# Optimization experiments

Measured on AMD Instinct MI355X. Metric: run time of the kernel, lower is better.

The kernel has to match this reference:

```python
import jax, jax.numpy as jnp
import numpy as np

B, T, TS, J, D, H = 4, 512, 512, 17, 256, 8
CD = D // H
SCALE = CD ** -0.5


def setup_inputs() -> dict:
    key = jax.random.key(0)
    ks = jax.random.split(key, 7)
    return {
        "q": jax.random.normal(ks[0], (B, T, J, D), dtype=jnp.float32),
        "kv": jax.random.normal(ks[1], (B, TS, J, D), dtype=jnp.float32),
        "Wq": jax.random.normal(ks[2], (D, D), dtype=jnp.float32) * (D ** -0.5),
        "Wk": jax.random.normal(ks[3], (D, D), dtype=jnp.float32) * (D ** -0.5),
        "Wv": jax.random.normal(ks[4], (D, D), dtype=jnp.float32) * (D ** -0.5),
        "Wp": jax.random.normal(ks[5], (D, D), dtype=jnp.float32) * (D ** -0.5),
        "bp": jnp.zeros((D,), dtype=jnp.float32),
    }


def reference(q, kv, Wq, Wk, Wv, Wp, bp):
    b, t, j, d = q.shape
    t_sup = kv.shape[1]
    h, cd = H, CD
    # linear projections (torch Linear: x @ W^T), split heads -> [b,h,j,t,cd]
    qh = (q @ Wq.T).reshape(b, t, j, h, cd).transpose(0, 3, 2, 1, 4)
    kh = (kv @ Wk.T).reshape(b, t_sup, j, h, cd).transpose(0, 3, 2, 1, 4)
    vh = (kv @ Wv.T).reshape(b, t_sup, j, h, cd).transpose(0, 3, 2, 1, 4)
    # full attention matrix over temporal axes: [b,h,j,t,t_sup]
    scores = jnp.einsum("bhjtc,bhjsc->bhjts", qh, kh) * SCALE
    attn = jax.nn.softmax(scores, axis=-1)
    out = jnp.einsum("bhjts,bhjsc->bhjtc", attn, vh)
    out = out.transpose(0, 3, 2, 1, 4).reshape(b, t, j, d)  # [b,t,j,d]
    return out @ Wp.T + bp
```

## Files before the change

### kernel.cpp

```cpp
#include <hip/hip_runtime.h>
#include <hip/hip_bf16.h>

#define BB 4
#define TT 512
#define JJ 17
#define DD 256
#define HH 8
#define MROWS (BB*TT*JJ)
#define SZE ((size_t)MROWS * DD)
#define WSZ (DD*DD)
#define QSCALE 0.2550265247510319f

typedef short v8s __attribute__((ext_vector_type(8)));
typedef float v4f __attribute__((ext_vector_type(4)));

__device__ __forceinline__ unsigned short f2bf(float f) {
    union { float f; unsigned int u; } c; c.f = f;
    unsigned int u = c.u;
    return (unsigned short)((u + 0x7FFF + ((u >> 16) & 1)) >> 16);
}
__device__ __forceinline__ unsigned int pkbf(float lo, float hi) {
    union { float f; unsigned int u; } a, b; a.f = lo; b.f = hi;
    return __builtin_amdgcn_perm(b.u + 0x8000u, a.u + 0x8000u, 0x07060302u);
}

__global__ __launch_bounds__(256) void prep_kernel(
    const float* __restrict__ q, const float* __restrict__ kv,
    const float* __restrict__ Wq, const float* __restrict__ Wk,
    const float* __restrict__ Wv, const float* __restrict__ Wp,
    unsigned short* __restrict__ qb, unsigned short* __restrict__ kvb,
    unsigned short* __restrict__ Wqb, unsigned short* __restrict__ Wkb,
    unsigned short* __restrict__ Wvb, unsigned short* __restrict__ Wpb)
{
    size_t i = ((size_t)blockIdx.x * 256 + threadIdx.x) * 8;
    const float* src; unsigned short* dst; size_t off; float scale = 1.f;
    if (i < SZE)            { src = q;  dst = qb;  off = i;        scale = QSCALE; }
    else if (i < 2 * SZE)   { src = kv; dst = kvb; off = i - SZE; }
    else {
        size_t k = i - 2 * SZE;
        int w = (int)(k >> 16);
        off = k & (WSZ - 1);
        src = (w == 0) ? Wq : (w == 1) ? Wk : (w == 2) ? Wv : Wp;
        dst = (w == 0) ? Wqb : (w == 1) ? Wkb : (w == 2) ? Wvb : Wpb;
    }
    float4 x0 = *(const float4*)(src + off);
    float4 x1 = *(const float4*)(src + off + 4);
    union { unsigned short s[8]; int4 v; } u;
    u.s[0] = f2bf(x0.x * scale); u.s[1] = f2bf(x0.y * scale);
    u.s[2] = f2bf(x0.z * scale); u.s[3] = f2bf(x0.w * scale);
    u.s[4] = f2bf(x1.x * scale); u.s[5] = f2bf(x1.y * scale);
    u.s[6] = f2bf(x1.z * scale); u.s[7] = f2bf(x1.w * scale);
    *(int4*)(dst + off) = u.v;
}

__global__ __launch_bounds__(256) void gemm_kernel(
    const unsigned short* __restrict__ A0,
    const unsigned short* __restrict__ A1,
    const unsigned short* __restrict__ A2,
    const unsigned short* __restrict__ W0,
    const unsigned short* __restrict__ W1,
    const unsigned short* __restrict__ W2,
    unsigned short* __restrict__ Y0,
    unsigned short* __restrict__ Y1,
    unsigned short* __restrict__ Y2,
    const float* __restrict__ bias,
    float* __restrict__ outf,
    int fp32out)
{
    const int z = blockIdx.z;
    const unsigned short* A = (z == 0) ? A0 : (z == 1) ? A1 : A2;
    const unsigned short* W = (z == 0) ? W0 : (z == 1) ? W1 : W2;
    unsigned short* Y       = (z == 0) ? Y0 : (z == 1) ? Y1 : Y2;

    const int bm = blockIdx.x;
    const int bn = blockIdx.y;

    __shared__ unsigned short As[128 * 40];
    __shared__ unsigned short Bs[128 * 40];

    const int tid  = threadIdx.x;
    const int wave = tid >> 6;
    const int lane = tid & 63;
    const int wm   = wave & 1;
    const int wn   = wave >> 1;
    const int quad = lane >> 4;
    const int l16  = lane & 15;

    const int colg = quad;
    int srow[2];
    srow[0] = wave * 16 + l16;
    srow[1] = srow[0] + 64;

    v4f acc[4][4] = {};

    for (int kt = 0; kt < 8; ++kt) {
        const int k0 = kt * 32;
        __syncthreads();
        #pragma unroll
        for (int c = 0; c < 2; ++c) {
            *(int4*)(&As[srow[c] * 40 + colg * 8]) =
                *(const int4*)(A + (size_t)(bm * 128 + srow[c]) * 256 + k0 + colg * 8);
            *(int4*)(&Bs[srow[c] * 40 + colg * 8]) =
                *(const int4*)(W + (size_t)(bn * 128 + srow[c]) * 256 + k0 + colg * 8);
        }
        __syncthreads();

        v8s a[4], b[4];
        #pragma unroll
        for (int i = 0; i < 4; ++i)
            a[i] = *(const v8s*)(&As[(wm * 64 + i * 16 + l16) * 40 + quad * 8]);
        #pragma unroll
        for (int j = 0; j < 4; ++j)
            b[j] = *(const v8s*)(&Bs[(wn * 64 + j * 16 + l16) * 40 + quad * 8]);
        #pragma unroll
        for (int i = 0; i < 4; ++i)
            #pragma unroll
            for (int j = 0; j < 4; ++j)
                acc[i][j] = __builtin_amdgcn_mfma_f32_16x16x32_bf16(
                    a[i], b[j], acc[i][j], 0, 0, 0);
    }

    #pragma unroll
    for (int i = 0; i < 4; ++i) {
        #pragma unroll
        for (int j = 0; j < 4; ++j) {
            #pragma unroll
            for (int r = 0; r < 4; ++r) {
                int gm = bm * 128 + wm * 64 + i * 16 + quad * 4 + r;
                int gn = bn * 128 + wn * 64 + j * 16 + l16;
                float v = acc[i][j][r];
                if (fp32out)
                    outf[(size_t)gm * 256 + gn] = v + bias[gn];
                else
                    Y[(size_t)gm * 256 + gn] = f2bf(v);
            }
        }
    }
}

#define VST 136
#define PST 72

__global__ __launch_bounds__(256) void attn_kernel(
    const unsigned short* __restrict__ Qp,
    const unsigned short* __restrict__ Kp,
    const unsigned short* __restrict__ Vp,
    unsigned short* __restrict__ Att)
{
    const int bjh = blockIdx.x;
    const int qt  = blockIdx.y;
    const int h   = bjh & 7;
    const int bj  = bjh >> 3;
    const int j   = bj % 17;
    const int b_  = bj / 17;

    __shared__ unsigned short Ks[128 * 40];
    __shared__ unsigned short Vs[32 * VST];
    __shared__ unsigned short Ps[128 * PST];
    __shared__ float Ls[128];

    const int tid  = threadIdx.x;
    const int wave = tid >> 6;
    const int lane = tid & 63;
    const int quad = lane >> 4;
    const int l16  = lane & 15;

    v8s qa[2];
    #pragma unroll
    for (int fi = 0; fi < 2; ++fi)
        qa[fi] = *(const v8s*)(
            Qp + ((size_t)(b_ * 512 + qt * 128 + wave * 32 + fi * 16 + l16) * 17 + j) * 256
               + h * 32 + quad * 8);

    float lacc[2] = {0.f, 0.f};
    v4f accO[2][2] = {};

    for (int kc = 0; kc < 4; ++kc) {
        __syncthreads();
        #pragma unroll
        for (int c = 0; c < 2; ++c) {
            int krow = wave * 16 + l16 + c * 64;
            *(int4*)(&Ks[krow * 40 + quad * 8]) = *(const int4*)(
                Kp + ((size_t)(b_ * 512 + kc * 128 + krow) * 17 + j) * 256 + h * 32 + quad * 8);
        }
        #pragma unroll
        for (int c = 0; c < 2; ++c) {
            int idx  = c * 256 + tid;
            int srow = idx >> 2;
            int cd0  = (idx & 3) << 3;
            int xof  = (((srow >> 3) ^ (cd0 >> 3)) << 3) + (srow & 7);
            union { int4 v; unsigned short s[8]; } u;
            u.v = *(const int4*)(
                Vp + ((size_t)(b_ * 512 + kc * 128 + srow) * 17 + j) * 256 + h * 32 + cd0);
            #pragma unroll
            for (int i = 0; i < 8; ++i)
                Vs[(cd0 + i) * VST + xof] = u.s[i];
        }
        __syncthreads();

        #pragma unroll
        for (int half = 0; half < 2; ++half) {
            v4f accST[4][2] = {};
            #pragma unroll
            for (int si = 0; si < 4; ++si) {
                v8s kb = *(const v8s*)(&Ks[((half * 4 + si) * 16 + l16) * 40 + quad * 8]);
                #pragma unroll
                for (int fi = 0; fi < 2; ++fi)
                    accST[si][fi] = __builtin_amdgcn_mfma_f32_16x16x32_bf16(
                        kb, qa[fi], accST[si][fi], 0, 0, 0);
            }
            #pragma unroll
            for (int fi = 0; fi < 2; ++fi) {
                int prow = (wave * 32 + fi * 16 + l16) * PST;
                #pragma unroll
                for (int si = 0; si < 4; ++si) {
                    float p0 = exp2f(accST[si][fi][0]);
                    float p1 = exp2f(accST[si][fi][1]);
                    float p2 = exp2f(accST[si][fi][2]);
                    float p3 = exp2f(accST[si][fi][3]);
                    lacc[fi] += (p0 + p1) + (p2 + p3);
                    uint2 pk;
                    pk.x = pkbf(p0, p1);
                    pk.y = pkbf(p2, p3);
                    *(uint2*)(&Ps[prow + si * 16 + quad * 4]) = pk;
                }
            }
            asm volatile("s_waitcnt lgkmcnt(0)" ::: "memory");

            #pragma unroll
            for (int ks = 0; ks < 2; ++ks) {
                v8s pa[2];
                #pragma unroll
                for (int fi = 0; fi < 2; ++fi)
                    pa[fi] = *(const v8s*)(&Ps[(wave * 32 + fi * 16 + l16) * PST +
                                               ks * 32 + quad * 8]);
                #pragma unroll
                for (int nj = 0; nj < 2; ++nj) {
                    int cd  = nj * 16 + l16;
                    int blk = (half * 8 + ks * 4 + quad) ^ (cd >> 3);
                    v8s vb = *(const v8s*)(&Vs[cd * VST + (blk << 3)]);
                    #pragma unroll
                    for (int fi = 0; fi < 2; ++fi)
                        accO[fi][nj] = __builtin_amdgcn_mfma_f32_16x16x32_bf16(
                            pa[fi], vb, accO[fi][nj], 0, 0, 0);
                }
            }
        }
    }

    #pragma unroll
    for (int fi = 0; fi < 2; ++fi) {
        float lv = lacc[fi];
        lv += __shfl_xor(lv, 16);
        lv += __shfl_xor(lv, 32);
        if (quad == 0) Ls[wave * 32 + fi * 16 + l16] = lv;
    }
    asm volatile("s_waitcnt lgkmcnt(0)" ::: "memory");

    #pragma unroll
    for (int fi = 0; fi < 2; ++fi) {
        float4 lv = *(float4*)(&Ls[wave * 32 + fi * 16 + quad * 4]);
        float rl[4] = {1.f / lv.x, 1.f / lv.y, 1.f / lv.z, 1.f / lv.w};
        #pragma unroll
        for (int nj = 0; nj < 2; ++nj) {
            #pragma unroll
            for (int r = 0; r < 4; ++r) {
                int trow = qt * 128 + wave * 32 + fi * 16 + quad * 4 + r;
                int cd   = nj * 16 + l16;
                float v  = accO[fi][nj][r] * rl[r];
                Att[((size_t)(b_ * 512 + trow) * 17 + j) * 256 + h * 32 + cd] = f2bf(v);
            }
        }
    }
}

extern "C" void kernel_launch(void* const* d_in, const int* in_sizes, int n_in,
                              void* d_out, int out_size, void* d_ws, size_t ws_size,
                              hipStream_t stream) {
    const float* q  = (const float*)d_in[0];
    const float* kv = (const float*)d_in[1];
    const float* Wq = (const float*)d_in[2];
    const float* Wk = (const float*)d_in[3];
    const float* Wv = (const float*)d_in[4];
    const float* Wp = (const float*)d_in[5];
    const float* bp = (const float*)d_in[6];

    unsigned short* ws  = (unsigned short*)d_ws;
    unsigned short* Qp  = ws;
    unsigned short* Kp  = ws + SZE;
    unsigned short* Vp  = ws + 2 * SZE;
    unsigned short* qb  = ws + 3 * SZE;
    unsigned short* kvb = ws + 4 * SZE;
    unsigned short* Wqb = ws + 5 * SZE;
    unsigned short* Wkb = Wqb + WSZ;
    unsigned short* Wvb = Wkb + WSZ;
    unsigned short* Wpb = Wvb + WSZ;
    unsigned short* Att = qb;
    float* out = (float*)d_out;

    prep_kernel<<<8832, 256, 0, stream>>>(q, kv, Wq, Wk, Wv, Wp,
                                          qb, kvb, Wqb, Wkb, Wvb, Wpb);
    gemm_kernel<<<dim3(272, 2, 3), 256, 0, stream>>>(
        qb, kvb, kvb, Wqb, Wkb, Wvb, Qp, Kp, Vp, nullptr, nullptr, 0);
    attn_kernel<<<dim3(544, 4, 1), 256, 0, stream>>>(Qp, Kp, Vp, Att);
    gemm_kernel<<<dim3(272, 2, 1), 256, 0, stream>>>(
        Att, Att, Att, Wpb, Wpb, Wpb, nullptr, nullptr, nullptr, bp, out, 1);
}
```

Measured before the change: 240.9 us.

## Double-buffer GEMM tiles via direct global-to-LDS loads with full-N blocks

The projection GEMM now uses 512-thread blocks that each cover the full 256-column output, so the A tile is read once per row block instead of twice. Tiles are fetched with global_load_lds straight into double-buffered, XOR-swizzled shared memory, and the next K slice is prefetched while MFMAs run on the current one. This is meant to cut redundant A traffic, register staging and barrier stalls. The cost is half as many blocks, higher LDS use per block, and reliance on the swizzle to avoid bank conflicts now that the row padding is gone.

```diff
diff --git a/kernel.cpp b/kernel.cpp
--- a/kernel.cpp
+++ b/kernel.cpp
@@ -22,6 +22,13 @@
 __device__ __forceinline__ unsigned int pkbf(float lo, float hi) {
     union { float f; unsigned int u; } a, b; a.f = lo; b.f = hi;
     return __builtin_amdgcn_perm(b.u + 0x8000u, a.u + 0x8000u, 0x07060302u);
+}
+
+__device__ __forceinline__ void gld16(const unsigned short* g, unsigned short* l) {
+    __builtin_amdgcn_global_load_lds(
+        (const __attribute__((address_space(1))) void*)g,
+        (__attribute__((address_space(3))) void*)l,
+        16, 0, 0);
 }
 
 __global__ __launch_bounds__(256) void prep_kernel(
@@ -53,7 +60,7 @@
     *(int4*)(dst + off) = u.v;
 }
 
-__global__ __launch_bounds__(256) void gemm_kernel(
+__global__ __launch_bounds__(512) void gemm_kernel(
     const unsigned short* __restrict__ A0,
     const unsigned short* __restrict__ A1,
     const unsigned short* __restrict__ A2,
@@ -67,57 +74,68 @@
     float* __restrict__ outf,
     int fp32out)
 {
-    const int z = blockIdx.z;
+    const int z = blockIdx.y;
     const unsigned short* A = (z == 0) ? A0 : (z == 1) ? A1 : A2;
     const unsigned short* W = (z == 0) ? W0 : (z == 1) ? W1 : W2;
     unsigned short* Y       = (z == 0) ? Y0 : (z == 1) ? Y1 : Y2;
 
     const int bm = blockIdx.x;
-    const int bn = blockIdx.y;
-
-    __shared__ unsigned short As[128 * 40];
-    __shared__ unsigned short Bs[128 * 40];
+
+    __shared__ unsigned short As[2][128 * 32];
+    __shared__ unsigned short Bs[2][256 * 32];
 
     const int tid  = threadIdx.x;
-    const int wave = tid >> 6;
+    const int wv   = tid >> 6;
     const int lane = tid & 63;
-    const int wm   = wave & 1;
-    const int wn   = wave >> 1;
+    const int wm   = wv & 1;
+    const int wn   = wv >> 1;
     const int quad = lane >> 4;
     const int l16  = lane & 15;
 
-    const int colg = quad;
-    int srow[2];
-    srow[0] = wave * 16 + l16;
-    srow[1] = srow[0] + 64;
+    const int s     = lane >> 2;
+    const int chunk = lane & 3;
+    const int fsw   = (s ^ (s >> 2)) & 3;
+    const int cg    = chunk ^ fsw;
+    const int srow  = wv * 16 + s;
+    const unsigned short* gA  = A + (size_t)(bm * 128 + srow) * 256 + cg * 8;
+    const unsigned short* gB0 = W + (size_t)srow * 256 + cg * 8;
+    const unsigned short* gB1 = W + (size_t)(128 + srow) * 256 + cg * 8;
+    unsigned short* lA  = &As[0][wv * 512 + lane * 8];
+    unsigned short* lB0 = &Bs[0][wv * 512 + lane * 8];
+    unsigned short* lB1 = &Bs[0][4096 + wv * 512 + lane * 8];
+
+    const int rch8 = (quad ^ ((l16 ^ (l16 >> 2)) & 3)) * 8;
 
     v4f acc[4][4] = {};
 
+    gld16(gA,  lA);
+    gld16(gB0, lB0);
+    gld16(gB1, lB1);
+    __syncthreads();
+
     for (int kt = 0; kt < 8; ++kt) {
-        const int k0 = kt * 32;
-        __syncthreads();
-        #pragma unroll
-        for (int c = 0; c < 2; ++c) {
-            *(int4*)(&As[srow[c] * 40 + colg * 8]) =
-                *(const int4*)(A + (size_t)(bm * 128 + srow[c]) * 256 + k0 + colg * 8);
-            *(int4*)(&Bs[srow[c] * 40 + colg * 8]) =
-                *(const int4*)(W + (size_t)(bn * 128 + srow[c]) * 256 + k0 + colg * 8);
-        }
-        __syncthreads();
-
+        const int cur = kt & 1;
+        if (kt < 7) {
+            const int nk = (kt + 1) * 32;
+            const int nb = cur ^ 1;
+            gld16(gA  + nk, lA  + nb * 4096);
+            gld16(gB0 + nk, lB0 + nb * 8192);
+            gld16(gB1 + nk, lB1 + nb * 8192);
+        }
         v8s a[4], b[4];
         #pragma unroll
         for (int i = 0; i < 4; ++i)
-            a[i] = *(const v8s*)(&As[(wm * 64 + i * 16 + l16) * 40 + quad * 8]);
+            a[i] = *(const v8s*)(&As[cur][(wm * 64 + i * 16 + l16) * 32 + rch8]);
         #pragma unroll
         for (int j = 0; j < 4; ++j)
-            b[j] = *(const v8s*)(&Bs[(wn * 64 + j * 16 + l16) * 40 + quad * 8]);
+            b[j] = *(const v8s*)(&Bs[cur][(wn * 64 + j * 16 + l16) * 32 + rch8]);
         #pragma unroll
         for (int i = 0; i < 4; ++i)
             #pragma unroll
             for (int j = 0; j < 4; ++j)
                 acc[i][j] = __builtin_amdgcn_mfma_f32_16x16x32_bf16(
                     a[i], b[j], acc[i][j], 0, 0, 0);
+        __syncthreads();
     }
 
     #pragma unroll
@@ -127,7 +145,7 @@
             #pragma unroll
             for (int r = 0; r < 4; ++r) {
                 int gm = bm * 128 + wm * 64 + i * 16 + quad * 4 + r;
-                int gn = bn * 128 + wn * 64 + j * 16 + l16;
+                int gn = wn * 64 + j * 16 + l16;
                 float v = acc[i][j][r];
                 if (fp32out)
                     outf[(size_t)gm * 256 + gn] = v + bias[gn];
@@ -300,9 +318,9 @@
 
     prep_kernel<<<8832, 256, 0, stream>>>(q, kv, Wq, Wk, Wv, Wp,
                                           qb, kvb, Wqb, Wkb, Wvb, Wpb);
-    gemm_kernel<<<dim3(272, 2, 3), 256, 0, stream>>>(
+    gemm_kernel<<<dim3(272, 3), 512, 0, stream>>>(
         qb, kvb, kvb, Wqb, Wkb, Wvb, Qp, Kp, Vp, nullptr, nullptr, 0);
     attn_kernel<<<dim3(544, 4, 1), 256, 0, stream>>>(Qp, Kp, Vp, Att);
-    gemm_kernel<<<dim3(272, 2, 1), 256, 0, stream>>>(
+    gemm_kernel<<<dim3(272, 1), 512, 0, stream>>>(
         Att, Att, Att, Wpb, Wpb, Wpb, nullptr, nullptr, nullptr, bp, out, 1);
 }
```

Measured after the change: 226.6 us. -6.0%, faster.
